# Optimization experiments

Hardware: AMD Instinct MI355X
Metric: run time of the kernel (lower is better)

Reference implementation:

```python
import jax, jax.numpy as jnp
import numpy as np

N = 100_000      # nodes
E = 1_600_000    # edges (before self-loops)
IN = 128         # in_channels
HID = 32         # hidden_channels
HEADS = 2        # attention heads
OUT = 64         # out_channels
NEG_SLOPE = 0.2  # PyG GATConv leaky-relu slope


def setup_inputs() -> dict:
    key = jax.random.key(0)
    ks = jax.random.split(key, 16)
    HC = HID * HEADS

    def glorot(k, shape, fan_in):
        return jax.random.normal(k, shape, jnp.float32) / np.sqrt(fan_in)

    return {
        "x": jax.random.normal(ks[0], (N, IN), jnp.float32),
        "edge_index": jax.random.randint(ks[1], (2, E), 0, N, jnp.int64),
        # layer 1: IN -> HID per head, concat
        "W1": glorot(ks[2], (IN, HC), IN),
        "as1": glorot(ks[3], (HEADS, HID), HID),
        "ad1": glorot(ks[4], (HEADS, HID), HID),
        "b1": jnp.zeros((HC,), jnp.float32),
        # layer 2: HC -> HID per head, concat
        "W2": glorot(ks[5], (HC, HC), HC),
        "as2": glorot(ks[6], (HEADS, HID), HID),
        "ad2": glorot(ks[7], (HEADS, HID), HID),
        "b2": jnp.zeros((HC,), jnp.float32),
        # layer 3: HC -> OUT, 1 head, no concat
        "W3": glorot(ks[8], (HC, OUT), HC),
        "as3": glorot(ks[9], (1, OUT), OUT),
        "ad3": glorot(ks[10], (1, OUT), OUT),
        "b3": jnp.zeros((OUT,), jnp.float32),
    }


def gat_conv(x, src, dst, W, a_src, a_dst, b, heads, out_ch, concat, n):
    # per-head linear transform: [n, heads, out_ch]
    h = (x @ W).reshape(n, heads, out_ch)
    # per-node attention logits: [n, heads]
    al_src = jnp.einsum('nhc,hc->nh', h, a_src)
    al_dst = jnp.einsum('nhc,hc->nh', h, a_dst)
    # raw edge scores with leaky relu: [e, heads]
    e = al_src[src] + al_dst[dst]
    e = jnp.where(e >= 0, e, NEG_SLOPE * e)
    # segment softmax over incoming edges of each dst node
    m = jax.ops.segment_max(e, dst, num_segments=n)          # [n, heads]
    ee = jnp.exp(e - m[dst])
    denom = jax.ops.segment_sum(ee, dst, num_segments=n)     # [n, heads]
    alpha = ee / denom[dst]
    # weighted scatter-add of source features
    out = jax.ops.segment_sum(h[src] * alpha[..., None], dst, num_segments=n)
    if concat:
        out = out.reshape(n, heads * out_ch)
    else:
        out = out.mean(axis=1)
    return out + b


def reference(x, edge_index, W1, as1, ad1, b1, W2, as2, ad2, b2, W3, as3, ad3, b3):
    # PyG GATConv adds self-loops by default
    loop = jnp.arange(N, dtype=edge_index.dtype)
    src = jnp.concatenate([edge_index[0], loop])
    dst = jnp.concatenate([edge_index[1], loop])

    h = gat_conv(x, src, dst, W1, as1, ad1, b1, HEADS, HID, True, N)
    h = jax.nn.relu(h)
    h = gat_conv(h, src, dst, W2, as2, ad2, b2, HEADS, HID, True, N)
    h = jax.nn.relu(h)
    out = gat_conv(h, src, dst, W3, as3, ad3, b3, 1, OUT, False, N)
    return out
```

## Files before the change

### kernel.cpp

```cpp
#include <hip/hip_runtime.h>
#include <hip/hip_fp16.h>

#define IN_CH   128
#define HC      64
#define NEG_SLOPE 0.2f

#define BSH   9
#define NPB   512
#define EPB   8192
#define DBIN  64

typedef __attribute__((ext_vector_type(8))) _Float16 f16x8;
typedef __attribute__((ext_vector_type(4))) float    f32x4;

__global__ __launch_bounds__(256) void wpack3_k(const float* __restrict__ W1, const float* __restrict__ W2,
                                                const float* __restrict__ W3, _Float16* __restrict__ P1,
                                                _Float16* __restrict__ P2, _Float16* __restrict__ P3,
                                                int* __restrict__ zeroz) {
    int o = blockIdx.x * 256 + threadIdx.x;
    if (o < 320) zeroz[o] = 0;
    const float* W; _Float16* P; int oo;
    if (o < 8192)       { W = W1; P = P1; oo = o; }
    else if (o < 12288) { W = W2; P = P2; oo = o - 8192; }
    else                { W = W3; P = P3; oo = o - 12288; }
    int j = oo & 7, l = (oo >> 3) & 63, t = (oo >> 9) & 3, s = oo >> 11;
    int row = s * 32 + ((l >> 4) << 3) + j;
    int col = (t << 4) + (l & 15);
    P[oo] = (_Float16)W[row * 64 + col];
}

__global__ __launch_bounds__(256) void csortA1_k(const int* __restrict__ ei, int* __restrict__ bcnt, int E) {
    __shared__ int cnt[256];
    cnt[threadIdx.x] = 0;
    __syncthreads();
    int base = blockIdx.x * EPB;
#pragma unroll
    for (int k = 0; k < EPB / 256; k++) {
        int i = base + k * 256 + threadIdx.x;
        if (i < E) atomicAdd(&cnt[ei[E + i] >> BSH], 1);
    }
    __syncthreads();
    int c = cnt[threadIdx.x];
    if (c) atomicAdd(&bcnt[threadIdx.x], c);
}

__global__ __launch_bounds__(256) void bscan_k(const int* __restrict__ bcnt, int* __restrict__ bbase,
                                               int* __restrict__ bcur, int nbuck, int E) {
    __shared__ int s[256];
    int tid = threadIdx.x;
    int v = (tid < nbuck) ? bcnt[tid] : 0;
    s[tid] = v; __syncthreads();
    for (int o = 1; o < 256; o <<= 1) {
        int t = (tid >= o) ? s[tid - o] : 0;
        __syncthreads();
        s[tid] += t;
        __syncthreads();
    }
    int ex = s[tid] - v;
    if (tid < nbuck) { bbase[tid] = ex; bcur[tid] = ex; }
    if (tid == 0) bbase[nbuck] = E;
}

__global__ __launch_bounds__(256) void csortA3_k(const int* __restrict__ ei, int* __restrict__ bcur,
                                                 unsigned* __restrict__ pairs, int E) {
    __shared__ int cnt[256];
    __shared__ int cur[256];
    cnt[threadIdx.x] = 0;
    __syncthreads();
    int base = blockIdx.x * EPB;
#pragma unroll
    for (int k = 0; k < EPB / 256; k++) {
        int i = base + k * 256 + threadIdx.x;
        if (i < E) atomicAdd(&cnt[ei[E + i] >> BSH], 1);
    }
    __syncthreads();
    int c = cnt[threadIdx.x];
    cur[threadIdx.x] = c ? atomicAdd(&bcur[threadIdx.x], c) : 0;
    __syncthreads();
#pragma unroll
    for (int k = 0; k < EPB / 256; k++) {
        int i = base + k * 256 + threadIdx.x;
        if (i < E) {
            int d = ei[E + i];
            int s = ei[i];
            int p = atomicAdd(&cur[d >> BSH], 1);
            pairs[p] = ((unsigned)(d & (NPB - 1)) << 17) | (unsigned)s;
        }
    }
}

__global__ __launch_bounds__(256) void csortB2_k(const unsigned* __restrict__ pairs, const int* __restrict__ bbase,
                                                 int* __restrict__ off, int* __restrict__ csr,
                                                 int* __restrict__ dcnt, int N, int E, int nbuck) {
    __shared__ int cnt[NPB];
    __shared__ int cur[NPB];
    __shared__ int ps[256];
    __shared__ int dh[DBIN];
    int b = blockIdx.x;
    int tid = threadIdx.x;
    int rs = bbase[b];
    int re = bbase[b + 1];

    cnt[tid] = 0; cnt[tid + 256] = 0;
    if (tid < DBIN) dh[tid] = 0;
    __syncthreads();
    for (int j = rs + tid; j < re; j += 256)
        atomicAdd(&cnt[pairs[j] >> 17], 1);
    __syncthreads();

    int c0 = cnt[2 * tid], c1 = cnt[2 * tid + 1];
    int n0 = b * NPB + 2 * tid;
    if (n0 < N)     atomicAdd(&dh[min(c0, DBIN - 1)], 1);
    if (n0 + 1 < N) atomicAdd(&dh[min(c1, DBIN - 1)], 1);
    int pair = c0 + c1;
    ps[tid] = pair;
    __syncthreads();
    for (int o = 1; o < 256; o <<= 1) {
        int t = (tid >= o) ? ps[tid - o] : 0;
        __syncthreads();
        ps[tid] += t;
        __syncthreads();
    }
    int base0 = rs + ps[tid] - pair;
    cur[2 * tid] = base0;
    cur[2 * tid + 1] = base0 + c0;
    if (n0 < N)     off[n0] = base0;
    if (n0 + 1 < N) off[n0 + 1] = base0 + c0;
    if (b == nbuck - 1 && tid == 0) off[N] = E;
    if (b == nbuck - 1 && tid < 64) csr[E + tid] = 0;
    __syncthreads();
    if (tid < DBIN && dh[tid]) atomicAdd(&dcnt[tid], dh[tid]);

    for (int j = rs + tid; j < re; j += 256) {
        unsigned v = pairs[j];
        int p = atomicAdd(&cur[v >> 17], 1);
        csr[p] = (int)(v & 0x1FFFF);
    }
}

__global__ void dscan_k(const int* __restrict__ dcnt, int* __restrict__ dcur) {
    __shared__ int s[DBIN];
    int tid = threadIdx.x;
    int v = dcnt[tid];
    s[tid] = v; __syncthreads();
    for (int o = 1; o < DBIN; o <<= 1) {
        int t = (tid >= o) ? s[tid - o] : 0;
        __syncthreads();
        s[tid] += t;
        __syncthreads();
    }
    dcur[tid] = s[tid] - v;
}

__global__ __launch_bounds__(256) void drank2_k(const int* __restrict__ off, int* __restrict__ dcur,
                                                int* __restrict__ perm, int N) {
    __shared__ int h[DBIN];
    __shared__ int cur[DBIN];
    int b = blockIdx.x, tid = threadIdx.x;
    if (tid < DBIN) h[tid] = 0;
    __syncthreads();
    int n0 = b * NPB + tid, n1 = n0 + 256;
    int d0 = -1, d1 = -1;
    if (n0 < N) { d0 = min(off[n0 + 1] - off[n0], DBIN - 1); atomicAdd(&h[d0], 1); }
    if (n1 < N) { d1 = min(off[n1 + 1] - off[n1], DBIN - 1); atomicAdd(&h[d1], 1); }
    __syncthreads();
    if (tid < DBIN) cur[tid] = h[tid] ? atomicAdd(&dcur[tid], h[tid]) : 0;
    __syncthreads();
    if (n0 < N) perm[atomicAdd(&cur[d0], 1)] = n0;
    if (n1 < N) perm[atomicAdd(&cur[d1], 1)] = n1;
}

template<int K, int HEADS, bool F16IN>
__global__ __launch_bounds__(256) void gemm_mfma_k(const void* __restrict__ Xv, const _Float16* __restrict__ P,
                                                   const float* __restrict__ a_s, const float* __restrict__ a_d,
                                                   __half* __restrict__ H, float* __restrict__ ALS,
                                                   float* __restrict__ ALD, int n) {
    __shared__ _Float16 lh[4][16 * 72];
    int tid = threadIdx.x;
    int wv = tid >> 6, lane = tid & 63;
    int wid = blockIdx.x * 4 + wv;
    int rowbase = wid << 4;
    if (rowbase >= n) return;
    int q = lane >> 4, cl = lane & 15;

    f16x8 b[K / 32][4];
    const f16x8* Pv = (const f16x8*)P;
#pragma unroll
    for (int s = 0; s < K / 32; s++)
#pragma unroll
        for (int t = 0; t < 4; t++)
            b[s][t] = Pv[(s * 4 + t) * 64 + lane];

    f32x4 c[4];
#pragma unroll
    for (int t = 0; t < 4; t++) c[t] = (f32x4){0.f, 0.f, 0.f, 0.f};

#pragma unroll
    for (int s = 0; s < K / 32; s++) {
        f16x8 a;
        if (F16IN) {
            const _Float16* xrow = (const _Float16*)Xv + (size_t)(rowbase + cl) * K + q * 8;
            a = *(const f16x8*)(xrow + s * 32);
        } else {
            const float* xrow = (const float*)Xv + (size_t)(rowbase + cl) * K + q * 8;
            float4 x0 = *(const float4*)(xrow + s * 32);
            float4 x1 = *(const float4*)(xrow + s * 32 + 4);
            a[0] = (_Float16)x0.x; a[1] = (_Float16)x0.y; a[2] = (_Float16)x0.z; a[3] = (_Float16)x0.w;
            a[4] = (_Float16)x1.x; a[5] = (_Float16)x1.y; a[6] = (_Float16)x1.z; a[7] = (_Float16)x1.w;
        }
#pragma unroll
        for (int t = 0; t < 4; t++)
            c[t] = __builtin_amdgcn_mfma_f32_16x16x32_f16(a, b[s][t], c[t], 0, 0, 0);
    }

    if (HEADS == 2) {
        float as0 = a_s[cl], as1 = a_s[16 + cl], as2 = a_s[32 + cl], as3 = a_s[48 + cl];
        float ad0 = a_d[cl], ad1 = a_d[16 + cl], ad2 = a_d[32 + cl], ad3 = a_d[48 + cl];
#pragma unroll
        for (int reg = 0; reg < 4; reg++) {
            float s0 = c[0][reg] * as0 + c[1][reg] * as1;
            float d0 = c[0][reg] * ad0 + c[1][reg] * ad1;
            float s1 = c[2][reg] * as2 + c[3][reg] * as3;
            float d1 = c[2][reg] * ad2 + c[3][reg] * ad3;
#pragma unroll
            for (int m = 1; m <= 8; m <<= 1) {
                s0 += __shfl_xor(s0, m, 64);
                d0 += __shfl_xor(d0, m, 64);
                s1 += __shfl_xor(s1, m, 64);
                d1 += __shfl_xor(d1, m, 64);
            }
            if (cl == 0) {
                int row = rowbase + q * 4 + reg;
                ALS[row * 2]     = s0;
                ALS[row * 2 + 1] = s1;
                ALD[row * 2]     = d0;
                ALD[row * 2 + 1] = d1;
            }
        }
    } else {
        float as0 = a_s[cl], as1 = a_s[16 + cl], as2 = a_s[32 + cl], as3 = a_s[48 + cl];
        float ad0 = a_d[cl], ad1 = a_d[16 + cl], ad2 = a_d[32 + cl], ad3 = a_d[48 + cl];
#pragma unroll
        for (int reg = 0; reg < 4; reg++) {
            float s0 = c[0][reg] * as0 + c[1][reg] * as1 + c[2][reg] * as2 + c[3][reg] * as3;
            float d0 = c[0][reg] * ad0 + c[1][reg] * ad1 + c[2][reg] * ad2 + c[3][reg] * ad3;
#pragma unroll
            for (int m = 1; m <= 8; m <<= 1) {
                s0 += __shfl_xor(s0, m, 64);
                d0 += __shfl_xor(d0, m, 64);
            }
            if (cl == 0) {
                int row = rowbase + q * 4 + reg;
                ALS[row] = s0;
                ALD[row] = d0;
            }
        }
    }

    _Float16* L = lh[wv];
#pragma unroll
    for (int t = 0; t < 4; t++)
#pragma unroll
        for (int reg = 0; reg < 4; reg++)
            L[(q * 4 + reg) * 72 + t * 16 + cl] = (_Float16)c[t][reg];
    __builtin_amdgcn_s_waitcnt(0);
    int rr = lane >> 2, seg = lane & 3;
    uint4 v0 = *(const uint4*)((const char*)L + rr * 144 + seg * 32);
    uint4 v1 = *(const uint4*)((const char*)L + rr * 144 + seg * 32 + 16);
    char* hb = (char*)(H + (size_t)rowbase * 64);
    *(uint4*)(hb + rr * 128 + seg * 32)      = v0;
    *(uint4*)(hb + rr * 128 + seg * 32 + 16) = v1;
}

template<int HEADS, int RELU, bool OUTF16>
__global__ __launch_bounds__(256) void aggregate_k(const __half* __restrict__ H, const float* __restrict__ ALS,
                                                   const float* __restrict__ ALD, const int* __restrict__ off,
                                                   const int* __restrict__ csr, const int* __restrict__ perm,
                                                   const float* __restrict__ bias, void* __restrict__ OUT, int n) {
    int lane = threadIdx.x & 63;
    int wv   = threadIdx.x >> 6;
    int c8   = lane & 7;
    int idx  = blockIdx.x * 32 + wv * 8 + (lane >> 3);
    bool alive = idx < n;
    int dst = perm[alive ? idx : 0];
    int head = (HEADS == 2) ? (c8 >> 2) : 0;

    int b0 = off[dst];
    int len = alive ? (off[dst + 1] - b0) : 0;
    float ald = ALD[dst * HEADS + head];

    float e = ALS[dst * HEADS + head] + ald;
    e = fmaxf(e, NEG_SLOPE * e);
    float ee = alive ? __expf(e) : 0.f;
    float den = ee;
    const uint4* Ho = (const uint4*)H;
    uint4 hv = Ho[dst * 8 + c8];
    float acc[8];
    {
        float2 p0 = __half22float2(*(const __half2*)&hv.x);
        float2 p1 = __half22float2(*(const __half2*)&hv.y);
        float2 p2 = __half22float2(*(const __half2*)&hv.z);
        float2 p3 = __half22float2(*(const __half2*)&hv.w);
        acc[0] = ee * p0.x; acc[1] = ee * p0.y; acc[2] = ee * p1.x; acc[3] = ee * p1.y;
        acc[4] = ee * p2.x; acc[5] = ee * p2.y; acc[6] = ee * p3.x; acc[7] = ee * p3.y;
    }

    int lmax = max(len, __shfl_xor(len, 8, 64));
    lmax = max(lmax, __shfl_xor(lmax, 16, 64));
    lmax = max(lmax, __shfl_xor(lmax, 32, 64));

    int j = 0;
    for (; j + 7 < lmax; j += 8) {
        int i0 = b0 + j;
        int s[8];
#pragma unroll
        for (int k = 0; k < 8; k++) s[k] = csr[i0 + k];
        float al[8];
#pragma unroll
        for (int k = 0; k < 8; k++) al[k] = ALS[s[k] * HEADS + head];
        uint4 h[8];
#pragma unroll
        for (int k = 0; k < 8; k++) h[k] = Ho[s[k] * 8 + c8];
#pragma unroll
        for (int k = 0; k < 8; k++) {
            float ek = al[k] + ald;
            ek = fmaxf(ek, NEG_SLOPE * ek);
            float wk = (j + k < len) ? __expf(ek) : 0.f;
            den += wk;
            float2 p0 = __half22float2(*(const __half2*)&h[k].x);
            float2 p1 = __half22float2(*(const __half2*)&h[k].y);
            float2 p2 = __half22float2(*(const __half2*)&h[k].z);
            float2 p3 = __half22float2(*(const __half2*)&h[k].w);
            acc[0] += wk * p0.x; acc[1] += wk * p0.y; acc[2] += wk * p1.x; acc[3] += wk * p1.y;
            acc[4] += wk * p2.x; acc[5] += wk * p2.y; acc[6] += wk * p3.x; acc[7] += wk * p3.y;
        }
    }
    for (; j < lmax; j++) {
        int s0 = csr[b0 + j];
        float alv = ALS[s0 * HEADS + head];
        uint4 h0 = Ho[s0 * 8 + c8];
        float e0 = alv + ald;
        e0 = fmaxf(e0, NEG_SLOPE * e0);
        float w0 = (j < len) ? __expf(e0) : 0.f;
        den += w0;
        float2 p0 = __half22float2(*(const __half2*)&h0.x);
        float2 p1 = __half22float2(*(const __half2*)&h0.y);
        float2 p2 = __half22float2(*(const __half2*)&h0.z);
        float2 p3 = __half22float2(*(const __half2*)&h0.w);
        acc[0] += w0 * p0.x; acc[1] += w0 * p0.y; acc[2] += w0 * p1.x; acc[3] += w0 * p1.y;
        acc[4] += w0 * p2.x; acc[5] += w0 * p2.y; acc[6] += w0 * p3.x; acc[7] += w0 * p3.y;
    }

    if (alive) {
        float4 b0v = ((const float4*)bias)[2 * c8];
        float4 b1v = ((const float4*)bias)[2 * c8 + 1];
        float rd = 1.f / den;
        float o[8];
        o[0] = acc[0] * rd + b0v.x; o[1] = acc[1] * rd + b0v.y;
        o[2] = acc[2] * rd + b0v.z; o[3] = acc[3] * rd + b0v.w;
        o[4] = acc[4] * rd + b1v.x; o[5] = acc[5] * rd + b1v.y;
        o[6] = acc[6] * rd + b1v.z; o[7] = acc[7] * rd + b1v.w;
        if (RELU) {
#pragma unroll
            for (int k = 0; k < 8; k++) o[k] = fmaxf(o[k], 0.f);
        }
        if (OUTF16) {
            __half2 q0 = __floats2half2_rn(o[0], o[1]);
            __half2 q1 = __floats2half2_rn(o[2], o[3]);
            __half2 q2 = __floats2half2_rn(o[4], o[5]);
            __half2 q3 = __floats2half2_rn(o[6], o[7]);
            uint4 u;
            u.x = *(unsigned*)&q0; u.y = *(unsigned*)&q1;
            u.z = *(unsigned*)&q2; u.w = *(unsigned*)&q3;
            ((uint4*)OUT)[dst * 8 + c8] = u;
        } else {
            ((float4*)OUT)[dst * 16 + 2 * c8]     = make_float4(o[0], o[1], o[2], o[3]);
            ((float4*)OUT)[dst * 16 + 2 * c8 + 1] = make_float4(o[4], o[5], o[6], o[7]);
        }
    }
}

extern "C" void kernel_launch(void* const* d_in, const int* in_sizes, int n_in,
                              void* d_out, int out_size, void* d_ws, size_t ws_size,
                              hipStream_t stream) {
    const float* x   = (const float*)d_in[0];
    const int*   ei  = (const int*)  d_in[1];
    const float* W1  = (const float*)d_in[2];
    const float* as1 = (const float*)d_in[3];
    const float* ad1 = (const float*)d_in[4];
    const float* b1  = (const float*)d_in[5];
    const float* W2  = (const float*)d_in[6];
    const float* as2 = (const float*)d_in[7];
    const float* ad2 = (const float*)d_in[8];
    const float* b2  = (const float*)d_in[9];
    const float* W3  = (const float*)d_in[10];
    const float* as3 = (const float*)d_in[11];
    const float* ad3 = (const float*)d_in[12];
    const float* b3  = (const float*)d_in[13];

    const int N = in_sizes[0] / IN_CH;
    const int E = in_sizes[1] / 2;
    const int NBUCK = (N + NPB - 1) >> BSH;
    const int NEB   = (E + EPB - 1) / EPB;

    char* p = (char*)d_ws;
    auto carve = [&](size_t bytes) {
        char* r = p;
        p += (bytes + 255) & ~(size_t)255;
        return r;
    };
    __half*    hbuf    = (__half*)   carve((size_t)N * HC * 2);
    __half*    obuf    = (__half*)   carve((size_t)N * HC * 2);
    float*     als     = (float*)    carve((size_t)N * 2 * 4);
    float*     ald     = (float*)    carve((size_t)N * 2 * 4);
    int*       off     = (int*)      carve((size_t)(N + 1) * 4);
    int*       csr     = (int*)      carve((size_t)(E + 64) * 4);
    unsigned*  pairs   = (unsigned*) carve((size_t)E * 4);
    int*       bcnt    = (int*)      carve((size_t)320 * 4);
    int*       dcnt    = bcnt + 256;
    int*       bbase   = (int*)      carve((size_t)260 * 4);
    int*       bcur    = (int*)      carve((size_t)256 * 4);
    int*       dcur    = (int*)      carve((size_t)DBIN * 4);
    int*       perm    = (int*)      carve((size_t)N * 4);
    _Float16*  wp1     = (_Float16*) carve((size_t)IN_CH * 64 * 2);
    _Float16*  wp2     = (_Float16*) carve((size_t)64 * 64 * 2);
    _Float16*  wp3     = (_Float16*) carve((size_t)64 * 64 * 2);

    const int NW8 = (N + 31) / 32;
    const int NBM = (N / 16 + 3) / 4;

    wpack3_k<<<64, 256, 0, stream>>>(W1, W2, W3, wp1, wp2, wp3, bcnt);

    csortA1_k<<<NEB, 256, 0, stream>>>(ei, bcnt, E);
    bscan_k  <<<1, 256, 0, stream>>>(bcnt, bbase, bcur, NBUCK, E);
    csortA3_k<<<NEB, 256, 0, stream>>>(ei, bcur, pairs, E);
    csortB2_k<<<NBUCK, 256, 0, stream>>>(pairs, bbase, off, csr, dcnt, N, E, NBUCK);

    dscan_k  <<<1, DBIN, 0, stream>>>(dcnt, dcur);
    drank2_k <<<NBUCK, 256, 0, stream>>>(off, dcur, perm, N);

    gemm_mfma_k<128, 2, false><<<NBM, 256, 0, stream>>>(x, wp1, as1, ad1, hbuf, als, ald, N);
    aggregate_k<2, 1, true>   <<<NW8, 256, 0, stream>>>(hbuf, als, ald, off, csr, perm, b1, obuf, N);

    gemm_mfma_k<64, 2, true><<<NBM, 256, 0, stream>>>(obuf, wp2, as2, ad2, hbuf, als, ald, N);
    aggregate_k<2, 1, true> <<<NW8, 256, 0, stream>>>(hbuf, als, ald, off, csr, perm, b2, obuf, N);

    gemm_mfma_k<64, 1, true><<<NBM, 256, 0, stream>>>(obuf, wp3, as3, ad3, hbuf, als, ald, N);
    aggregate_k<1, 0, false><<<NW8, 256, 0, stream>>>(hbuf, als, ald, off, csr, perm, b3, d_out, N);
}
```

Baseline: 330.0 us.

## Halve CSR sort bucket size and cache per-block bucket counts between passes

Shrinks the destination bucket from 512 to 256 nodes and halves edges per block, which doubles the number of blocks in the edge-sort and CSR-building kernels for more parallelism. The first counting pass now stores its per-block bucket histogram to global memory, so the scatter pass reads it instead of recounting, avoiding a second read of the destination array and the shared atomics that went with it. In exchange it adds a counts buffer, moves the bucket scan to 512 threads, and makes the global bucket atomics more contended.

```diff
diff --git a/kernel.cpp b/kernel.cpp
--- a/kernel.cpp
+++ b/kernel.cpp
@@ -5,9 +5,9 @@
 #define HC      64
 #define NEG_SLOPE 0.2f
 
-#define BSH   9
-#define NPB   512
-#define EPB   8192
+#define BSH   8
+#define NPB   256
+#define EPB   4096
 #define DBIN  64
 
 typedef __attribute__((ext_vector_type(8))) _Float16 f16x8;
@@ -18,7 +18,7 @@
                                                 _Float16* __restrict__ P2, _Float16* __restrict__ P3,
                                                 int* __restrict__ zeroz) {
     int o = blockIdx.x * 256 + threadIdx.x;
-    if (o < 320) zeroz[o] = 0;
+    if (o < 576) zeroz[o] = 0;
     const float* W; _Float16* P; int oo;
     if (o < 8192)       { W = W1; P = P1; oo = o; }
     else if (o < 12288) { W = W2; P = P2; oo = o - 8192; }
@@ -29,28 +29,35 @@
     P[oo] = (_Float16)W[row * 64 + col];
 }
 
-__global__ __launch_bounds__(256) void csortA1_k(const int* __restrict__ ei, int* __restrict__ bcnt, int E) {
-    __shared__ int cnt[256];
-    cnt[threadIdx.x] = 0;
+__global__ __launch_bounds__(256) void csortA1_k(const int* __restrict__ ei, int* __restrict__ bcnt,
+                                                 int* __restrict__ countsT, int E) {
+    __shared__ int cnt[512];
+    int tid = threadIdx.x;
+    cnt[tid] = 0; cnt[tid + 256] = 0;
     __syncthreads();
     int base = blockIdx.x * EPB;
 #pragma unroll
     for (int k = 0; k < EPB / 256; k++) {
-        int i = base + k * 256 + threadIdx.x;
+        int i = base + k * 256 + tid;
         if (i < E) atomicAdd(&cnt[ei[E + i] >> BSH], 1);
     }
     __syncthreads();
-    int c = cnt[threadIdx.x];
-    if (c) atomicAdd(&bcnt[threadIdx.x], c);
-}
-
-__global__ __launch_bounds__(256) void bscan_k(const int* __restrict__ bcnt, int* __restrict__ bbase,
+#pragma unroll
+    for (int r = 0; r < 2; r++) {
+        int b = r * 256 + tid;
+        int c = cnt[b];
+        countsT[blockIdx.x * 512 + b] = c;
+        if (c) atomicAdd(&bcnt[b], c);
+    }
+}
+
+__global__ __launch_bounds__(512) void bscan_k(const int* __restrict__ bcnt, int* __restrict__ bbase,
                                                int* __restrict__ bcur, int nbuck, int E) {
-    __shared__ int s[256];
-    int tid = threadIdx.x;
-    int v = (tid < nbuck) ? bcnt[tid] : 0;
+    __shared__ int s[512];
+    int tid = threadIdx.x;
+    int v = bcnt[tid];
     s[tid] = v; __syncthreads();
-    for (int o = 1; o < 256; o <<= 1) {
+    for (int o = 1; o < 512; o <<= 1) {
         int t = (tid >= o) ? s[tid - o] : 0;
         __syncthreads();
         s[tid] += t;
@@ -61,25 +68,21 @@
     if (tid == 0) bbase[nbuck] = E;
 }
 
-__global__ __launch_bounds__(256) void csortA3_k(const int* __restrict__ ei, int* __restrict__ bcur,
-                                                 unsigned* __restrict__ pairs, int E) {
-    __shared__ int cnt[256];
-    __shared__ int cur[256];
-    cnt[threadIdx.x] = 0;
+__global__ __launch_bounds__(256) void csortA3_k(const int* __restrict__ ei, const int* __restrict__ countsT,
+                                                 int* __restrict__ bcur, unsigned* __restrict__ pairs, int E) {
+    __shared__ int cur[512];
+    int tid = threadIdx.x;
+#pragma unroll
+    for (int r = 0; r < 2; r++) {
+        int b = r * 256 + tid;
+        int c = countsT[blockIdx.x * 512 + b];
+        cur[b] = c ? atomicAdd(&bcur[b], c) : 0;
+    }
     __syncthreads();
     int base = blockIdx.x * EPB;
 #pragma unroll
     for (int k = 0; k < EPB / 256; k++) {
-        int i = base + k * 256 + threadIdx.x;
-        if (i < E) atomicAdd(&cnt[ei[E + i] >> BSH], 1);
-    }
-    __syncthreads();
-    int c = cnt[threadIdx.x];
-    cur[threadIdx.x] = c ? atomicAdd(&bcur[threadIdx.x], c) : 0;
-    __syncthreads();
-#pragma unroll
-    for (int k = 0; k < EPB / 256; k++) {
-        int i = base + k * 256 + threadIdx.x;
+        int i = base + k * 256 + tid;
         if (i < E) {
             int d = ei[E + i];
             int s = ei[i];
@@ -101,19 +104,17 @@
     int rs = bbase[b];
     int re = bbase[b + 1];
 
-    cnt[tid] = 0; cnt[tid + 256] = 0;
+    cnt[tid] = 0;
     if (tid < DBIN) dh[tid] = 0;
     __syncthreads();
     for (int j = rs + tid; j < re; j += 256)
         atomicAdd(&cnt[pairs[j] >> 17], 1);
     __syncthreads();
 
-    int c0 = cnt[2 * tid], c1 = cnt[2 * tid + 1];
-    int n0 = b * NPB + 2 * tid;
-    if (n0 < N)     atomicAdd(&dh[min(c0, DBIN - 1)], 1);
-    if (n0 + 1 < N) atomicAdd(&dh[min(c1, DBIN - 1)], 1);
-    int pair = c0 + c1;
-    ps[tid] = pair;
+    int c0 = cnt[tid];
+    int n0 = b * NPB + tid;
+    if (n0 < N) atomicAdd(&dh[min(c0, DBIN - 1)], 1);
+    ps[tid] = c0;
     __syncthreads();
     for (int o = 1; o < 256; o <<= 1) {
         int t = (tid >= o) ? ps[tid - o] : 0;
@@ -121,11 +122,9 @@
         ps[tid] += t;
         __syncthreads();
     }
-    int base0 = rs + ps[tid] - pair;
-    cur[2 * tid] = base0;
-    cur[2 * tid + 1] = base0 + c0;
-    if (n0 < N)     off[n0] = base0;
-    if (n0 + 1 < N) off[n0 + 1] = base0 + c0;
+    int base0 = rs + ps[tid] - c0;
+    cur[tid] = base0;
+    if (n0 < N) off[n0] = base0;
     if (b == nbuck - 1 && tid == 0) off[N] = E;
     if (b == nbuck - 1 && tid < 64) csr[E + tid] = 0;
     __syncthreads();
@@ -159,15 +158,13 @@
     int b = blockIdx.x, tid = threadIdx.x;
     if (tid < DBIN) h[tid] = 0;
     __syncthreads();
-    int n0 = b * NPB + tid, n1 = n0 + 256;
-    int d0 = -1, d1 = -1;
+    int n0 = b * 256 + tid;
+    int d0 = -1;
     if (n0 < N) { d0 = min(off[n0 + 1] - off[n0], DBIN - 1); atomicAdd(&h[d0], 1); }
-    if (n1 < N) { d1 = min(off[n1 + 1] - off[n1], DBIN - 1); atomicAdd(&h[d1], 1); }
     __syncthreads();
     if (tid < DBIN) cur[tid] = h[tid] ? atomicAdd(&dcur[tid], h[tid]) : 0;
     __syncthreads();
     if (n0 < N) perm[atomicAdd(&cur[d0], 1)] = n0;
-    if (n1 < N) perm[atomicAdd(&cur[d1], 1)] = n1;
 }
 
 template<int K, int HEADS, bool F16IN>
@@ -416,12 +413,13 @@
     int*       off     = (int*)      carve((size_t)(N + 1) * 4);
     int*       csr     = (int*)      carve((size_t)(E + 64) * 4);
     unsigned*  pairs   = (unsigned*) carve((size_t)E * 4);
-    int*       bcnt    = (int*)      carve((size_t)320 * 4);
-    int*       dcnt    = bcnt + 256;
-    int*       bbase   = (int*)      carve((size_t)260 * 4);
-    int*       bcur    = (int*)      carve((size_t)256 * 4);
+    int*       bcnt    = (int*)      carve((size_t)576 * 4);
+    int*       dcnt    = bcnt + 512;
+    int*       bbase   = (int*)      carve((size_t)520 * 4);
+    int*       bcur    = (int*)      carve((size_t)512 * 4);
     int*       dcur    = (int*)      carve((size_t)DBIN * 4);
     int*       perm    = (int*)      carve((size_t)N * 4);
+    int*       countsT = (int*)      carve((size_t)NEB * 512 * 4);
     _Float16*  wp1     = (_Float16*) carve((size_t)IN_CH * 64 * 2);
     _Float16*  wp2     = (_Float16*) carve((size_t)64 * 64 * 2);
     _Float16*  wp3     = (_Float16*) carve((size_t)64 * 64 * 2);
@@ -431,9 +429,9 @@
 
     wpack3_k<<<64, 256, 0, stream>>>(W1, W2, W3, wp1, wp2, wp3, bcnt);
 
-    csortA1_k<<<NEB, 256, 0, stream>>>(ei, bcnt, E);
-    bscan_k  <<<1, 256, 0, stream>>>(bcnt, bbase, bcur, NBUCK, E);
-    csortA3_k<<<NEB, 256, 0, stream>>>(ei, bcur, pairs, E);
+    csortA1_k<<<NEB, 256, 0, stream>>>(ei, bcnt, countsT, E);
+    bscan_k  <<<1, 512, 0, stream>>>(bcnt, bbase, bcur, NBUCK, E);
+    csortA3_k<<<NEB, 256, 0, stream>>>(ei, countsT, bcur, pairs, E);
     csortB2_k<<<NBUCK, 256, 0, stream>>>(pairs, bbase, off, csr, dcnt, N, E, NBUCK);
 
     dscan_k  <<<1, DBIN, 0, stream>>>(dcnt, dcur);
```

Measured after the change: 332.0 us. No clear change (+0.6%).
